# Performance work log

Hardware: AMD Instinct MI355X
Metric: run time of the kernel (lower is better)

Reference implementation:

```python
import jax, jax.numpy as jnp
import numpy as np

TEMPERATURE = 0.07


def setup_inputs() -> dict:
    key = jax.random.key(0)
    k1, k2 = jax.random.split(key)
    B, D = 4096, 256
    x = jax.random.normal(k1, (B, D), dtype=jnp.float32)
    y = jax.random.normal(k2, (B, D), dtype=jnp.float32)
    # L2-normalize so dot products lie in [-1, 1] (realistic contrastive
    # embeddings; keeps exp(dot / 0.07) finite as the original code assumes).
    x = x / jnp.linalg.norm(x, axis=-1, keepdims=True)
    y = y / jnp.linalg.norm(y, axis=-1, keepdims=True)
    return {"x": x, "y": y}


def reference(x, y):
    # Faithful translation of the (quirky) original loop:
    # for each row i, neg_dot starts at zeros and is filled one j at a time;
    # at EVERY inner step k the code computes exp(neg_dot/T) over the full
    # vector (entries j>k are still 0 -> exp=1) and accumulates
    #   loss += -log(exp[i] / sum(exp)).
    # Vectorized:
    #   S[i,j] = x_i . y_j / T
    #   denom[i,k] = sum_{j<=k} exp(S[i,j]) + (B-1-k)    (zeros contribute e^0)
    #   numer log term: S[i,i] if k>=i else 0 -> contributes (B-i)*S[i,i]
    B = x.shape[0]
    S = jnp.einsum("id,jd->ij", x, y) / TEMPERATURE          # [B, B]
    cumE = jnp.cumsum(jnp.exp(S), axis=1)                     # [B, B]
    k = jnp.arange(B, dtype=S.dtype)
    denom = cumE + (B - 1.0 - k)[None, :]                     # [B, B]
    diag = jnp.diagonal(S)                                    # [B]
    n_hits = (B - jnp.arange(B)).astype(S.dtype)              # k >= i count
    loss = jnp.sum(jnp.log(denom)) - jnp.sum(n_hits * diag)
    return loss
```

## Files before the change

kernel.cpp:

```cpp
#include <hip/hip_runtime.h>

typedef __bf16  bf16x8 __attribute__((ext_vector_type(8)));
typedef short   s16x8  __attribute__((ext_vector_type(8)));
typedef float   f32x4  __attribute__((ext_vector_type(4)));
typedef unsigned short u16;
typedef u16     u16x4  __attribute__((ext_vector_type(4)));
typedef unsigned int u32;

#define B_SZ 4096
#define D_SZ 256

static constexpr float SCALE = (float)(1.4426950408889634 / 0.07);
static constexpr float LN2F  = 0.69314718055994531f;

__device__ __forceinline__ u16 f2bf(float f) {
  unsigned u = __float_as_uint(f);
  unsigned r = u + 0x7FFFu + ((u >> 16) & 1u);
  return (u16)(r >> 16);
}
__device__ __forceinline__ float bf2f(u16 h) {
  return __uint_as_float((u32)h << 16);
}

template<bool BF>
__device__ __forceinline__ bf16x8 ld8(const u16* pb, const float* pf) {
  if constexpr (BF) {
    return *(const bf16x8*)pb;
  } else {
    f32x4 a = *(const f32x4*)pf;
    f32x4 b = *(const f32x4*)(pf + 4);
    s16x8 s;
#pragma unroll
    for (int i = 0; i < 4; ++i) { s[i] = (short)f2bf(a[i]); s[i + 4] = (short)f2bf(b[i]); }
    return __builtin_bit_cast(bf16x8, s);
  }
}

__global__ __launch_bounds__(256) void cl_convert(const float* __restrict__ x,
                                                  const float* __restrict__ y,
                                                  u16* __restrict__ xb,
                                                  u16* __restrict__ yb) {
  const int idx = (int)(blockIdx.x * 256 + threadIdx.x) * 4;
  f32x4 vx = *(const f32x4*)(x + idx);
  f32x4 vy = *(const f32x4*)(y + idx);
  u16x4 sx, sy;
#pragma unroll
  for (int i = 0; i < 4; ++i) { sx[i] = f2bf(vx[i]); sy[i] = f2bf(vy[i]); }
  *(u16x4*)(xb + idx) = sx;
  *(u16x4*)(yb + idx) = sy;
}

__global__ __launch_bounds__(256, 2) void cl_gemm(const u16* __restrict__ xb,
                                                  const u16* __restrict__ yb,
                                                  u16* __restrict__ Sl) {
  __shared__ u16 As[2][128 * 64];
  __shared__ u16 Bs[2][128 * 64];
  const int tid  = threadIdx.x;
  const int lane = tid & 63;
  const int wv   = tid >> 6;
  const int l15  = lane & 15;
  const int lg   = lane >> 4;
  const int wm   = wv >> 1;
  const int wn   = wv & 1;
  int bid = (int)blockIdx.x;
  bid = (bid & 7) * 128 + (bid >> 3);
  const int brow = (bid >> 5) << 7;
  const int bcol = (bid & 31) << 7;

  auto stage_panel = [&](u16* panel, const u16* src, int row0, int kt) {
#pragma unroll
    for (int i = 0; i < 4; ++i) {
      const int chunk = i * 4 + wv;
      const int r = chunk * 8 + (lane >> 3);
      const int cs = ((lane & 7) << 4) ^ ((r & 7) << 4);
      const char* g = (const char*)src + ((size_t)(row0 + r) << 9) + (kt << 7) + cs;
      auto lp = (__attribute__((address_space(3))) u32*)
                  ((char*)panel + chunk * 1024 + lane * 16);
      __builtin_amdgcn_global_load_lds((const __attribute__((address_space(1))) u32*)g,
                                       lp, 16, 0, 0);
    }
  };

  f32x4 acc[4][4] = {};

  stage_panel(As[0], xb, brow, 0);
  stage_panel(Bs[0], yb, bcol, 0);
  __syncthreads();

#pragma unroll 1
  for (int kt = 0; kt < 4; ++kt) {
    if (kt < 3) {
      stage_panel(As[(kt + 1) & 1], xb, brow, kt + 1);
      stage_panel(Bs[(kt + 1) & 1], yb, bcol, kt + 1);
    }
    const u16* Ap = As[kt & 1];
    const u16* Bp = Bs[kt & 1];
    bf16x8 Af[4][2], Bf[4][2];
#pragma unroll
    for (int mi = 0; mi < 4; ++mi)
#pragma unroll
      for (int ks = 0; ks < 2; ++ks) {
        const int ra = (wm << 6) + (mi << 4) + l15;
        const int ca = ((ks << 6) + (lg << 4)) ^ ((ra & 7) << 4);
        Af[mi][ks] = *(const bf16x8*)((const char*)Ap + (ra << 7) + ca);
        const int rb = (wn << 6) + (mi << 4) + l15;
        const int cb = ((ks << 6) + (lg << 4)) ^ ((rb & 7) << 4);
        Bf[mi][ks] = *(const bf16x8*)((const char*)Bp + (rb << 7) + cb);
      }
#pragma unroll
    for (int mi = 0; mi < 4; ++mi)
#pragma unroll
      for (int ni = 0; ni < 4; ++ni)
#pragma unroll
        for (int ks = 0; ks < 2; ++ks)
          acc[mi][ni] = __builtin_amdgcn_mfma_f32_16x16x32_bf16(
              Af[mi][ks], Bf[ni][ks], acc[mi][ni], 0, 0, 0);
    __syncthreads();
  }

#pragma unroll
  for (int mi = 0; mi < 4; ++mi)
#pragma unroll
    for (int ni = 0; ni < 4; ++ni) {
      const int rg = brow + (wm << 6) + (mi << 4) + (lg << 2);
      const int cg = bcol + (wn << 6) + (ni << 4) + l15;
#pragma unroll
      for (int v = 0; v < 4; ++v)
        Sl[(size_t)(rg + v) * B_SZ + cg] = f2bf(acc[mi][ni][v] * SCALE);
    }
}

__global__ __launch_bounds__(256) void cl_scan(const u16* __restrict__ Sl,
                                               float* __restrict__ partials) {
  __shared__ float wtot[4];
  __shared__ float red[256];
  const int row  = (int)blockIdx.x;
  const int tid  = threadIdx.x;
  const int lane = tid & 63;
  const int wv   = tid >> 6;

  const u16* rp = Sl + (size_t)row * B_SZ + tid * 16;
  s16x8 a = *(const s16x8*)rp;
  s16x8 b = *(const s16x8*)(rp + 8);
  float t[16], p[16];
  float run = 0.f;
#pragma unroll
  for (int j = 0; j < 8; ++j) { t[j] = bf2f((u16)a[j]); t[8 + j] = bf2f((u16)b[j]); }
#pragma unroll
  for (int j = 0; j < 16; ++j) { run += __builtin_amdgcn_exp2f(t[j]); p[j] = run; }

  float s = run;
#pragma unroll
  for (int d = 1; d < 64; d <<= 1) {
    float u = __shfl_up(s, (unsigned)d, 64);
    if (lane >= d) s += u;
  }
  if (lane == 63) wtot[wv] = s;
  __syncthreads();
  float off = 0.f;
#pragma unroll
  for (int w = 0; w < 4; ++w) if (w < wv) off += wtot[w];
  const float excl = off + (s - run);

  float lacc = 0.f;
  const int c0 = tid * 16;
#pragma unroll
  for (int j = 0; j < 16; ++j)
    lacc += __builtin_amdgcn_logf(excl + p[j] + (float)(B_SZ - 1 - (c0 + j)));
  if ((row >> 4) == tid) lacc -= (float)(B_SZ - row) * t[row & 15];
  lacc *= LN2F;

  red[tid] = lacc;
  __syncthreads();
#pragma unroll
  for (int o = 128; o > 0; o >>= 1) {
    if (tid < o) red[tid] += red[tid + o];
    __syncthreads();
  }
  if (tid == 0) partials[row] = red[0];
}

__global__ __launch_bounds__(256) void cl_final(const float* __restrict__ p,
                                                float* __restrict__ out) {
  __shared__ float red[256];
  const int tid = threadIdx.x;
  float s = 0.f;
#pragma unroll
  for (int k = 0; k < 16; ++k) s += p[tid + 256 * k];
  red[tid] = s;
  __syncthreads();
#pragma unroll
  for (int o = 128; o > 0; o >>= 1) {
    if (tid < o) red[tid] += red[tid + o];
    __syncthreads();
  }
  if (tid == 0) out[0] = red[0];
}

template<bool BF>
__global__ __launch_bounds__(256) void cl_main(const float* __restrict__ x,
                                               const float* __restrict__ y,
                                               const u16* __restrict__ xb,
                                               const u16* __restrict__ yb,
                                               float* __restrict__ partials) {
  __shared__ float st[16][68];
  __shared__ float red[256];
  const int tid  = threadIdx.x;
  const int lane = tid & 63;
  const int wv   = tid >> 6;
  const int l15  = lane & 15;
  const int lg   = lane >> 4;
  const int i0   = blockIdx.x * 16;

  bf16x8 A[8];
  {
    const size_t base = (size_t)(i0 + l15) * D_SZ + (lg << 3);
#pragma unroll
    for (int ks = 0; ks < 8; ++ks)
      A[ks] = ld8<BF>(xb + base + ks * 32, x + base + ks * 32);
  }

  float lacc = 0.f, carry = 0.f;

  auto load_b = [&](bf16x8 (&F)[8], int t) {
    const size_t jb = (size_t)(t * 64 + (wv << 4) + l15) * D_SZ + (lg << 3);
#pragma unroll
    for (int ks = 0; ks < 8; ++ks)
      F[ks] = ld8<BF>(yb + jb + ks * 32, y + jb + ks * 32);
  };

  auto body = [&](bf16x8 (&F)[8], int t) {
    f32x4 acc = {0.f, 0.f, 0.f, 0.f};
#pragma unroll
    for (int ks = 0; ks < 8; ++ks)
      acc = __builtin_amdgcn_mfma_f32_16x16x32_bf16(A[ks], F[ks], acc, 0, 0, 0);
    __syncthreads();
    const int colg = t * 64 + (wv << 4) + l15;
#pragma unroll
    for (int v = 0; v < 4; ++v) {
      float tv = acc[v] * SCALE;
      const int rowl = (lg << 2) + v;
      if (i0 + rowl == colg) lacc -= (float)(B_SZ - colg) * tv;
      st[rowl][(wv << 4) + l15] = tv;
    }
    __syncthreads();
    const int row = (wv << 2) + lg;
    f32x4 tv4 = *(const f32x4*)&st[row][l15 << 2];
    float e0 = __builtin_amdgcn_exp2f(tv4[0]);
    float e1 = __builtin_amdgcn_exp2f(tv4[1]);
    float e2 = __builtin_amdgcn_exp2f(tv4[2]);
    float e3 = __builtin_amdgcn_exp2f(tv4[3]);
    float p1 = e0 + e1, p2 = p1 + e2, p3 = p2 + e3;
    float s = p3;
#pragma unroll
    for (int d = 1; d < 16; d <<= 1) {
      float u = __shfl_up(s, (unsigned)d, 16);
      if (l15 >= d) s += u;
    }
    const float base = carry + (s - p3);
    const float c0 = (float)(B_SZ - 1 - (t * 64 + (l15 << 2)));
    lacc += __builtin_amdgcn_logf(base + e0 + c0)
          + __builtin_amdgcn_logf(base + p1 + (c0 - 1.f))
          + __builtin_amdgcn_logf(base + p2 + (c0 - 2.f))
          + __builtin_amdgcn_logf(base + p3 + (c0 - 3.f));
    carry += __shfl(s, 15, 16);
  };

  bf16x8 B0[8], B1[8];
  load_b(B0, 0);
#pragma unroll 1
  for (int t2 = 0; t2 < 32; ++t2) {
    const int t0 = t2 * 2;
    load_b(B1, t0 + 1);
    body(B0, t0);
    if (t0 + 2 < 64) load_b(B0, t0 + 2);
    body(B1, t0 + 1);
  }

  red[tid] = lacc * LN2F;
  __syncthreads();
#pragma unroll
  for (int o = 128; o > 0; o >>= 1) {
    if (tid < o) red[tid] += red[tid + o];
    __syncthreads();
  }
  if (tid == 0) partials[blockIdx.x] = red[0];
}

__global__ __launch_bounds__(256) void cl_reduce(const float* __restrict__ p,
                                                 float* __restrict__ out) {
  __shared__ float red[256];
  const int tid = threadIdx.x;
  red[tid] = p[tid];
  __syncthreads();
#pragma unroll
  for (int o = 128; o > 0; o >>= 1) {
    if (tid < o) red[tid] += red[tid + o];
    __syncthreads();
  }
  if (tid == 0) out[0] = red[0];
}

extern "C" void kernel_launch(void* const* d_in, const int* in_sizes, int n_in,
                              void* d_out, int out_size, void* d_ws, size_t ws_size,
                              hipStream_t stream) {
  const float* x = (const float*)d_in[0];
  const float* y = (const float*)d_in[1];
  float* out = (float*)d_out;
  const size_t BD = (size_t)B_SZ * D_SZ;

  float* partials = (float*)d_ws;
  u16* xb = (u16*)((char*)d_ws + 16384);
  u16* yb = xb + BD;
  u16* Sl = yb + BD;
  const size_t need = 16384 + 4 * BD + 2 * (size_t)B_SZ * B_SZ;

  if (ws_size >= need) {
    cl_convert<<<(int)(BD / 1024), 256, 0, stream>>>(x, y, xb, yb);
    cl_gemm<<<1024, 256, 0, stream>>>(xb, yb, Sl);
    cl_scan<<<B_SZ, 256, 0, stream>>>(Sl, partials);
    cl_final<<<1, 256, 0, stream>>>(partials, out);
  } else {
    float* fpart = (float*)d_ws;
    u16* fxb = (u16*)((char*)d_ws + 4096);
    u16* fyb = fxb + BD;
    const size_t fneed = 4096 + 4 * BD;
    if (ws_size >= fneed) {
      cl_convert<<<(int)(BD / 1024), 256, 0, stream>>>(x, y, fxb, fyb);
      cl_main<true><<<B_SZ / 16, 256, 0, stream>>>(x, y, fxb, fyb, fpart);
    } else {
      cl_main<false><<<B_SZ / 16, 256, 0, stream>>>(x, y, fxb, fyb, fpart);
    }
    cl_reduce<<<1, 256, 0, stream>>>(fpart, out);
  }
}
```

Before: 37.83 us.

## Fuse final reduction into scan via atomic counter; transpose MFMA for vector stores

Swaps the MFMA operand order so each lane holds four consecutive columns of S. The epilogue can then write 4 bf16 values with one 8-byte store instead of four strided 2-byte stores. The scan kernel now reduces with wave shuffles instead of a shared-memory tree. The last block to finish, found through an atomic counter that cl_convert resets, does the final sum, so the separate cl_final launch is gone. This adds a threadfence and an atomic per block, and the result depends on the counter being reset correctly every call.

```diff
diff --git a/kernel.cpp b/kernel.cpp
--- a/kernel.cpp
+++ b/kernel.cpp
@@ -39,7 +39,9 @@
 __global__ __launch_bounds__(256) void cl_convert(const float* __restrict__ x,
                                                   const float* __restrict__ y,
                                                   u16* __restrict__ xb,
-                                                  u16* __restrict__ yb) {
+                                                  u16* __restrict__ yb,
+                                                  u32* __restrict__ cnt) {
+  if (blockIdx.x == 0 && threadIdx.x == 0) *cnt = 0u;
   const int idx = (int)(blockIdx.x * 256 + threadIdx.x) * 4;
   f32x4 vx = *(const f32x4*)(x + idx);
   f32x4 vy = *(const f32x4*)(y + idx);
@@ -114,7 +116,7 @@
 #pragma unroll
         for (int ks = 0; ks < 2; ++ks)
           acc[mi][ni] = __builtin_amdgcn_mfma_f32_16x16x32_bf16(
-              Af[mi][ks], Bf[ni][ks], acc[mi][ni], 0, 0, 0);
+              Bf[ni][ks], Af[mi][ks], acc[mi][ni], 0, 0, 0);
     __syncthreads();
   }
 
@@ -122,18 +124,22 @@
   for (int mi = 0; mi < 4; ++mi)
 #pragma unroll
     for (int ni = 0; ni < 4; ++ni) {
-      const int rg = brow + (wm << 6) + (mi << 4) + (lg << 2);
-      const int cg = bcol + (wn << 6) + (ni << 4) + l15;
-#pragma unroll
-      for (int v = 0; v < 4; ++v)
-        Sl[(size_t)(rg + v) * B_SZ + cg] = f2bf(acc[mi][ni][v] * SCALE);
+      u16x4 o;
+#pragma unroll
+      for (int v = 0; v < 4; ++v) o[v] = f2bf(acc[mi][ni][v] * SCALE);
+      const int rs = brow + (wm << 6) + (mi << 4) + l15;
+      const int cs = bcol + (wn << 6) + (ni << 4) + (lg << 2);
+      *(u16x4*)(Sl + (size_t)rs * B_SZ + cs) = o;
     }
 }
 
 __global__ __launch_bounds__(256) void cl_scan(const u16* __restrict__ Sl,
-                                               float* __restrict__ partials) {
+                                               float* __restrict__ partials,
+                                               u32* __restrict__ cnt,
+                                               float* __restrict__ out) {
   __shared__ float wtot[4];
-  __shared__ float red[256];
+  __shared__ float red2[4];
+  __shared__ int lastflag;
   const int row  = (int)blockIdx.x;
   const int tid  = threadIdx.x;
   const int lane = tid & 63;
@@ -170,31 +176,28 @@
   if ((row >> 4) == tid) lacc -= (float)(B_SZ - row) * t[row & 15];
   lacc *= LN2F;
 
-  red[tid] = lacc;
-  __syncthreads();
-#pragma unroll
-  for (int o = 128; o > 0; o >>= 1) {
-    if (tid < o) red[tid] += red[tid + o];
-    __syncthreads();
-  }
-  if (tid == 0) partials[row] = red[0];
-}
-
-__global__ __launch_bounds__(256) void cl_final(const float* __restrict__ p,
-                                                float* __restrict__ out) {
-  __shared__ float red[256];
-  const int tid = threadIdx.x;
-  float s = 0.f;
-#pragma unroll
-  for (int k = 0; k < 16; ++k) s += p[tid + 256 * k];
-  red[tid] = s;
-  __syncthreads();
-#pragma unroll
-  for (int o = 128; o > 0; o >>= 1) {
-    if (tid < o) red[tid] += red[tid + o];
-    __syncthreads();
-  }
-  if (tid == 0) out[0] = red[0];
+#pragma unroll
+  for (int d = 1; d < 64; d <<= 1) lacc += __shfl_xor(lacc, d, 64);
+  if (lane == 0) red2[wv] = lacc;
+  __syncthreads();
+  if (tid == 0) {
+    partials[row] = (red2[0] + red2[1]) + (red2[2] + red2[3]);
+    __threadfence();
+    u32 done = atomicAdd(cnt, 1u);
+    lastflag = (done == (u32)(gridDim.x - 1));
+  }
+  __syncthreads();
+  if (lastflag) {
+    __threadfence();
+    float fs = 0.f;
+#pragma unroll
+    for (int k = 0; k < 16; ++k) fs += partials[tid + 256 * k];
+#pragma unroll
+    for (int d = 1; d < 64; d <<= 1) fs += __shfl_xor(fs, d, 64);
+    if (lane == 0) red2[wv] = fs;
+    __syncthreads();
+    if (tid == 0) out[0] = (red2[0] + red2[1]) + (red2[2] + red2[3]);
+  }
 }
 
 template<bool BF>
@@ -310,23 +313,23 @@
   const size_t BD = (size_t)B_SZ * D_SZ;
 
   float* partials = (float*)d_ws;
-  u16* xb = (u16*)((char*)d_ws + 16384);
+  u32* cnt = (u32*)((char*)d_ws + 16384);
+  u16* xb = (u16*)((char*)d_ws + 16384 + 256);
   u16* yb = xb + BD;
   u16* Sl = yb + BD;
-  const size_t need = 16384 + 4 * BD + 2 * (size_t)B_SZ * B_SZ;
+  const size_t need = 16384 + 256 + 4 * BD + 2 * (size_t)B_SZ * B_SZ;
 
   if (ws_size >= need) {
-    cl_convert<<<(int)(BD / 1024), 256, 0, stream>>>(x, y, xb, yb);
+    cl_convert<<<(int)(BD / 1024), 256, 0, stream>>>(x, y, xb, yb, cnt);
     cl_gemm<<<1024, 256, 0, stream>>>(xb, yb, Sl);
-    cl_scan<<<B_SZ, 256, 0, stream>>>(Sl, partials);
-    cl_final<<<1, 256, 0, stream>>>(partials, out);
+    cl_scan<<<B_SZ, 256, 0, stream>>>(Sl, partials, cnt, out);
   } else {
     float* fpart = (float*)d_ws;
     u16* fxb = (u16*)((char*)d_ws + 4096);
     u16* fyb = fxb + BD;
     const size_t fneed = 4096 + 4 * BD;
     if (ws_size >= fneed) {
-      cl_convert<<<(int)(BD / 1024), 256, 0, stream>>>(x, y, fxb, fyb);
+      cl_convert<<<(int)(BD / 1024), 256, 0, stream>>>(x, y, fxb, fyb, (u32*)fpart);
       cl_main<true><<<B_SZ / 16, 256, 0, stream>>>(x, y, fxb, fyb, fpart);
     } else {
       cl_main<false><<<B_SZ / 16, 256, 0, stream>>>(x, y, fxb, fyb, fpart);
```

Result: slower. 122.7 us (+224.4%).
